# Kernel optimization log

Hardware: AMD Instinct MI355X
Metric: run time of the kernel (lower is better)

## Reference

```python
import jax, jax.numpy as jnp
import numpy as np

B, T_IN, T_OUT, C = 32, 512, 256, 64
NB_IN, NB_OUT = 16, 16
D = 128          # d_model
L = 3            # e_layers (hidden Siren layers before last)
E_IN = NB_IN * C
E_OUT = NB_OUT * C
LIN_IN = (NB_IN + 1) * C + 4
LIN_OUT = (NB_OUT + 1) * C


def _siren_params(key, E, w0_initial):
    ks = jax.random.split(key, 6)
    def unif(k, shape, std):
        return jax.random.uniform(k, shape, jnp.float32, -std, std)
    c6 = float(np.sqrt(6.0 / D))
    return dict(
        W0=unif(ks[0], (E, D, 1), 1.0),        # first layer: w_std = 1/dim_in, dim_in=1
        b0=unif(ks[1], (E, D), 1.0),
        Wh=unif(ks[2], (L - 1, E, D, D), c6),   # sqrt(6/dim)/w0, w0=1
        bh=unif(ks[3], (L - 1, E, D), c6),
        Wl=unif(ks[4], (E, 1, D), c6),
        bl=unif(ks[5], (E, 1), c6),
        w0i=w0_initial,                          # per-ensemble first-layer frequency
    )


def setup_inputs() -> dict:
    key = jax.random.key(0)
    ks = jax.random.split(key, 8)
    inp = {
        "x_enc": jax.random.normal(ks[0], (B, T_IN, C), jnp.float32),
        "x_mark_enc": jax.random.normal(ks[1], (B, T_IN, 4), jnp.float32),
        "x_dec": jax.random.normal(ks[2], (B, T_OUT, C), jnp.float32),
        "x_mark_dec": jax.random.normal(ks[3], (B, T_OUT, 4), jnp.float32),
    }
    # w0_initial: repeat(linspace(1, nb, nb), 'e -> (e c)')
    w0i_in = jnp.repeat(jnp.linspace(1.0, NB_IN, NB_IN, dtype=jnp.float32), C)
    w0i_out = jnp.repeat(jnp.linspace(1.0, NB_OUT, NB_OUT, dtype=jnp.float32), C)
    p_in = _siren_params(ks[4], E_IN, w0i_in)
    p_out = _siren_params(ks[5], E_OUT, w0i_out)
    for k, v in p_in.items():
        inp[k + "_in"] = v
    for k, v in p_out.items():
        inp[k + "_out"] = v
    std = float(1.0 / np.sqrt(LIN_IN))
    inp["Wlin"] = jax.random.uniform(ks[6], (LIN_OUT, LIN_IN), jnp.float32, -std, std)
    inp["blin"] = jax.random.uniform(ks[7], (LIN_OUT,), jnp.float32, -std, std)
    return inp


def _eigenfunc(T, nb, W0, b0, Wh, bh, Wl, bl, w0i):
    # SirenNet on domain [T,1] -> normalized eigenfunctions [T, nb+1, C]
    domain = jnp.linspace(0.0, 1.0, T, dtype=W0.dtype)[:, None]
    y = jnp.einsum('eoi,ti->teo', W0, domain) + b0           # [T,E,D]
    x = jnp.sin(w0i[None, :, None] * y)                       # Sine(w0_initial)
    for l in range(Wh.shape[0]):                              # hidden layers, w0 = 1
        x = jnp.sin(jnp.einsum('eoi,tei->teo', Wh[l], x) + bh[l])
    y = jnp.einsum('eoi,tei->teo', Wl, x) + bl                # [T,E,1], identity final act
    ef = y.reshape(T, nb, C)                                  # 't (e c) 1 -> t e c'
    ef = jnp.concatenate([jnp.ones((T, 1, C), ef.dtype), ef], axis=1)  # add_ones
    norm = jnp.sqrt(jnp.sum(ef * ef, axis=1, keepdims=True))  # normalize over basis dim
    return ef / norm


def reference(x_enc, x_mark_enc, x_dec, x_mark_dec,
              W0_in, b0_in, Wh_in, bh_in, Wl_in, bl_in, w0i_in,
              W0_out, b0_out, Wh_out, bh_out, Wl_out, bl_out, w0i_out,
              Wlin, blin):
    ef_in = _eigenfunc(T_IN, NB_IN, W0_in, b0_in, Wh_in, bh_in, Wl_in, bl_in, w0i_in)
    ef_out = _eigenfunc(T_OUT, NB_OUT, W0_out, b0_out, Wh_out, bh_out, Wl_out, bl_out, w0i_out)
    coeffs = jnp.einsum('btc,tec->bec', x_enc, ef_in)         # [B, nb+1, C]
    label = x_mark_enc[:, -1]                                  # [B, 4]
    flat = coeffs.reshape(coeffs.shape[0], -1)                 # 'b e c -> b (e c)'
    flat_in = jnp.concatenate([flat, label], axis=-1)
    pred = flat_in @ Wlin.T + blin                             # nn.Linear
    pred_coeff = pred.reshape(-1, NB_OUT + 1, C)
    pred_recon = jnp.einsum('bec,tec->btc', pred_coeff, ef_out)  # [B, pred_len, C]
    return pred_recon
```

## Files before the change

kernel.cpp:

```cpp
#include <hip/hip_runtime.h>
#include <hip/hip_bf16.h>
#include <math.h>


typedef short  bf16x8 __attribute__((ext_vector_type(8)));
typedef float  f32x4  __attribute__((ext_vector_type(4)));
typedef unsigned short u16;
typedef u16    u16x8  __attribute__((ext_vector_type(8)));
typedef unsigned int u32;
typedef u32    u32x4  __attribute__((ext_vector_type(4)));

constexpr int DD    = 128;
constexpr int E_TOT = 1024;
constexpr int T_INc = 512;
constexpr int T_OUTc= 256;
constexpr int BBc   = 32;
constexpr int CCc   = 64;
constexpr int NB1   = 17;
constexpr int EF_W  = NB1 * CCc;
constexpr int LIN_I = EF_W + 4;
constexpr int LIN_O = EF_W;

#define INV2PI 0.15915494309189535f

__device__ __forceinline__ float hsin(float rev) {
  return __builtin_amdgcn_sinf(rev);
}

__device__ __forceinline__ u32 pkrn(float a, float b) {
  __hip_bfloat162 h = __float22bfloat162_rn(float2{a, b});
  u32 r;
  __builtin_memcpy(&r, &h, 4);
  return r;
}

__device__ __forceinline__ int swz(int row, int col) {
  return row * DD + ((((col << 1) ^ ((row & 15) << 4)) >> 1));
}

__global__ __launch_bounds__(256, 4) void eigen_persist(
    const float* __restrict__ W0i, const float* __restrict__ b0i,
    const float* __restrict__ Whi, const float* __restrict__ bhi,
    const float* __restrict__ Wli, const float* __restrict__ bli,
    const float* __restrict__ w0ii, float* __restrict__ efni,
    const float* __restrict__ W0o, const float* __restrict__ b0o,
    const float* __restrict__ Who, const float* __restrict__ bho,
    const float* __restrict__ Wlo, const float* __restrict__ blo,
    const float* __restrict__ w0io, float* __restrict__ efno)
{
  __shared__ u16 xP[2][4096];
  __shared__ float yPart[4 * 32];
  __shared__ float w0s[128], b0s[128];

  const bool isIn = (blockIdx.x < E_TOT);
  const int  e    = blockIdx.x & (E_TOT - 1);
  const int  NIT  = isIn ? (T_INc / 32) : (T_OUTc / 32);
  const float tstep = isIn ? (1.0f / (float)(T_INc - 1)) : (1.0f / (float)(T_OUTc - 1));
  const float* W0 = isIn ? W0i : W0o;
  const float* b0 = isIn ? b0i : b0o;
  const float* Wh = isIn ? Whi : Who;
  const float* bh = isIn ? bhi : bho;
  const float* Wl = isIn ? Wli : Wlo;
  const float* bl = isIn ? bli : blo;
  const float* w0i = isIn ? w0ii : w0io;
  float* efn = isIn ? efni : efno;

  const int tid  = threadIdx.x;
  const int lane = tid & 63;
  const int wo   = tid >> 6;
  const int lm   = lane & 15;
  const int lg   = lane >> 4;

  const float wi  = w0i[e];
  const float blv = bl[e];

  if (tid < 128)       w0s[tid]       = W0[(size_t)e * DD + tid] * (wi * INV2PI);
  else if (tid < 256)  b0s[tid - 128] = b0[(size_t)e * DD + tid - 128] * (wi * INV2PI);

  float bhv[2][2], wlv[2];
  #pragma unroll
  for (int n = 0; n < 2; ++n) {
    const int o = wo * 32 + n * 16 + lm;
    bhv[0][n] = bh[(size_t)e * DD + o] * INV2PI;
    bhv[1][n] = bh[((size_t)E_TOT + e) * DD + o] * INV2PI;
    wlv[n]    = Wl[(size_t)e * DD + o];
  }

  bf16x8 wfrag[2][4][2];
  #pragma unroll
  for (int l = 0; l < 2; ++l) {
    const float* Wg = Wh + ((size_t)l * E_TOT + e) * (DD * DD);
    #pragma unroll
    for (int kk = 0; kk < 4; ++kk)
      #pragma unroll
      for (int n = 0; n < 2; ++n) {
        const float* p = Wg + (wo * 32 + n * 16 + lm) * DD + kk * 32 + lg * 8;
        const float4 a = *(const float4*)p;
        const float4 c = *(const float4*)(p + 4);
        u32x4 u;
        u[0] = pkrn(a.x, a.y);
        u[1] = pkrn(a.z, a.w);
        u[2] = pkrn(c.x, c.y);
        u[3] = pkrn(c.z, c.w);
        wfrag[l][kk][n] = __builtin_bit_cast(bf16x8, u);
      }
  }
  __syncthreads();

  const int tl = tid >> 3;
  const int q  = tid & 7;

  u16* x0p = xP[0];
  u16* x1p = xP[1];

  for (int it = 0; it < NIT; ++it) {
    {
      const float dom = (float)(it * 32 + tl) * tstep;
      #pragma unroll
      for (int c = 0; c < 2; ++c) {
        const int d = q * 16 + c * 8;
        const float4 wa = *(const float4*)&w0s[d];
        const float4 wb = *(const float4*)&w0s[d + 4];
        const float4 ba = *(const float4*)&b0s[d];
        const float4 bb = *(const float4*)&b0s[d + 4];
        u32x4 u;
        u[0] = pkrn(hsin(fmaf(wa.x, dom, ba.x)), hsin(fmaf(wa.y, dom, ba.y)));
        u[1] = pkrn(hsin(fmaf(wa.z, dom, ba.z)), hsin(fmaf(wa.w, dom, ba.w)));
        u[2] = pkrn(hsin(fmaf(wb.x, dom, bb.x)), hsin(fmaf(wb.y, dom, bb.y)));
        u[3] = pkrn(hsin(fmaf(wb.z, dom, bb.z)), hsin(fmaf(wb.w, dom, bb.w)));
        *(u16x8*)&x0p[swz(tl, d)] = __builtin_bit_cast(u16x8, u);
      }
    }
    __syncthreads();

    f32x4 acc[2][2];

    #pragma unroll
    for (int m = 0; m < 2; ++m)
      #pragma unroll
      for (int n = 0; n < 2; ++n) acc[m][n] = (f32x4){0.f, 0.f, 0.f, 0.f};
    #pragma unroll
    for (int kk = 0; kk < 4; ++kk) {
      const int kb = kk * 32 + lg * 8;
      bf16x8 ah[2];
      #pragma unroll
      for (int m = 0; m < 2; ++m)
        ah[m] = *(const bf16x8*)&x0p[swz(m * 16 + lm, kb)];
      #pragma unroll
      for (int m = 0; m < 2; ++m)
        #pragma unroll
        for (int n = 0; n < 2; ++n)
          acc[m][n] = __builtin_amdgcn_mfma_f32_16x16x32_bf16(ah[m], wfrag[0][kk][n], acc[m][n], 0, 0, 0);
    }
    #pragma unroll
    for (int m = 0; m < 2; ++m)
      #pragma unroll
      for (int n = 0; n < 2; ++n) {
        const int o = wo * 32 + n * 16 + lm;
        const int t = m * 16 + lg * 4;
        const u32 p0 = pkrn(hsin(fmaf(acc[m][n][0], INV2PI, bhv[0][n])),
                            hsin(fmaf(acc[m][n][1], INV2PI, bhv[0][n])));
        const u32 p1 = pkrn(hsin(fmaf(acc[m][n][2], INV2PI, bhv[0][n])),
                            hsin(fmaf(acc[m][n][3], INV2PI, bhv[0][n])));
        x1p[swz(t + 0, o)] = (u16)p0;
        x1p[swz(t + 1, o)] = (u16)(p0 >> 16);
        x1p[swz(t + 2, o)] = (u16)p1;
        x1p[swz(t + 3, o)] = (u16)(p1 >> 16);
      }
    __syncthreads();

    #pragma unroll
    for (int m = 0; m < 2; ++m)
      #pragma unroll
      for (int n = 0; n < 2; ++n) acc[m][n] = (f32x4){0.f, 0.f, 0.f, 0.f};
    #pragma unroll
    for (int kk = 0; kk < 4; ++kk) {
      const int kb = kk * 32 + lg * 8;
      bf16x8 ah[2];
      #pragma unroll
      for (int m = 0; m < 2; ++m)
        ah[m] = *(const bf16x8*)&x1p[swz(m * 16 + lm, kb)];
      #pragma unroll
      for (int m = 0; m < 2; ++m)
        #pragma unroll
        for (int n = 0; n < 2; ++n)
          acc[m][n] = __builtin_amdgcn_mfma_f32_16x16x32_bf16(ah[m], wfrag[1][kk][n], acc[m][n], 0, 0, 0);
    }

    #pragma unroll
    for (int m = 0; m < 2; ++m) {
      float p[4];
      #pragma unroll
      for (int r = 0; r < 4; ++r)
        p[r] = wlv[0] * hsin(fmaf(acc[m][0][r], INV2PI, bhv[1][0]))
             + wlv[1] * hsin(fmaf(acc[m][1][r], INV2PI, bhv[1][1]));
      #pragma unroll
      for (int r = 0; r < 4; ++r) {
        p[r] += __shfl_xor(p[r], 1);
        p[r] += __shfl_xor(p[r], 2);
        p[r] += __shfl_xor(p[r], 4);
        p[r] += __shfl_xor(p[r], 8);
      }
      if (lm == 0) {
        #pragma unroll
        for (int r = 0; r < 4; ++r)
          yPart[wo * 32 + m * 16 + lg * 4 + r] = p[r];
      }
    }
    __syncthreads();

    if (tid < 32) {
      const float s = yPart[tid] + yPart[32 + tid] + yPart[64 + tid] + yPart[96 + tid];
      efn[(size_t)(it * 32 + tid) * EF_W + CCc + e] = s + blv;
    }
  }
}

__global__ void normalize_all(float* __restrict__ efn_in, float* __restrict__ efn_out)
{
  const int tb = blockIdx.x;
  float* row = (tb < T_INc) ? (efn_in + (size_t)tb * EF_W)
                            : (efn_out + (size_t)(tb - T_INc) * EF_W);
  const int c = threadIdx.x;
  float v[16];
  float s = 1.0f;
  #pragma unroll
  for (int n = 0; n < 16; ++n) {
    v[n] = row[CCc + n * CCc + c];
    s += v[n] * v[n];
  }
  const float inv = 1.0f / sqrtf(s);
  row[c] = inv;
  #pragma unroll
  for (int n = 0; n < 16; ++n)
    row[CCc + n * CCc + c] = v[n] * inv;
}

__global__ __launch_bounds__(512) void coeffs_kernel(
    const float* __restrict__ x_enc, const float* __restrict__ x_mark_enc,
    const float* __restrict__ efn_in, float* __restrict__ flat_in)
{
  const int n  = blockIdx.x;
  const int b  = blockIdx.y;
  const int c  = threadIdx.x & 63;
  const int ch = threadIdx.x >> 6;
  __shared__ float red[8][64];
  float acc = 0.0f;
  #pragma unroll 4
  for (int t = ch * 64; t < ch * 64 + 64; ++t)
    acc += x_enc[((size_t)b * T_INc + t) * CCc + c]
         * efn_in[(size_t)t * EF_W + n * CCc + c];
  red[ch][c] = acc;
  __syncthreads();
  if (ch == 0) {
    #pragma unroll
    for (int k = 1; k < 8; ++k) acc += red[k][c];
    flat_in[b * LIN_I + n * CCc + c] = acc;
    if (n == 0 && c < 4)
      flat_in[b * LIN_I + EF_W + c] =
          x_mark_enc[((size_t)b * T_INc + (T_INc - 1)) * 4 + c];
  }
}

__global__ __launch_bounds__(256) void transpose_lin(const float* __restrict__ W,
                                                     float* __restrict__ Wt)
{
  __shared__ float tile[32][33];
  const int j0 = blockIdx.x * 32;
  const int o0 = blockIdx.y * 32;
  const int tx = threadIdx.x & 31, ty = threadIdx.x >> 5;
  #pragma unroll
  for (int r = 0; r < 32; r += 8) {
    const int o = o0 + ty + r, j = j0 + tx;
    tile[ty + r][tx] = (o < LIN_O && j < LIN_I) ? W[(size_t)o * LIN_I + j] : 0.f;
  }
  __syncthreads();
  #pragma unroll
  for (int r = 0; r < 32; r += 8) {
    const int j = j0 + ty + r, o = o0 + tx;
    if (j < LIN_I && o < LIN_O) Wt[(size_t)j * LIN_O + o] = tile[tx][ty + r];
  }
}

__global__ __launch_bounds__(256) void linear_t_kernel(
    const float* __restrict__ flat_in, const float* __restrict__ Wt,
    const float* __restrict__ blin, float* __restrict__ pred)
{
  const int og = blockIdx.x;
  const int b  = blockIdx.y;
  const int c  = threadIdx.x & 63;
  const int ch = threadIdx.x >> 6;
  const int o  = og * 64 + c;
  __shared__ float red[4][64];
  const float* xi = flat_in + b * LIN_I;
  float acc = 0.0f;
  #pragma unroll 4
  for (int j = ch * 273; j < ch * 273 + 273; ++j)
    acc += Wt[(size_t)j * LIN_O + o] * xi[j];
  red[ch][c] = acc;
  __syncthreads();
  if (ch == 0)
    pred[b * LIN_O + o] = acc + red[1][c] + red[2][c] + red[3][c] + blin[o];
}

__global__ void linear_row_kernel(const float* __restrict__ flat_in,
                                  const float* __restrict__ Wlin,
                                  const float* __restrict__ blin,
                                  float* __restrict__ pred)
{
  const int o = blockIdx.x * 64 + threadIdx.x;
  const int b = blockIdx.y;
  const float* w  = Wlin + (size_t)o * LIN_I;
  const float* xi = flat_in + b * LIN_I;
  float acc = blin[o];
  for (int j = 0; j < LIN_I; ++j) acc += w[j] * xi[j];
  pred[b * LIN_O + o] = acc;
}

__global__ void recon_kernel(const float* __restrict__ pred,
                             const float* __restrict__ efn_out,
                             float* __restrict__ out)
{
  const int b = blockIdx.y;
  const int t = blockIdx.x * 4 + (threadIdx.x >> 6);
  const int c = threadIdx.x & 63;
  float acc = 0.0f;
  #pragma unroll
  for (int n = 0; n < NB1; ++n)
    acc += pred[b * LIN_O + n * CCc + c]
         * efn_out[(size_t)t * EF_W + n * CCc + c];
  out[((size_t)b * T_OUTc + t) * CCc + c] = acc;
}

extern "C" void kernel_launch(void* const* d_in, const int* in_sizes, int n_in,
                              void* d_out, int out_size, void* d_ws, size_t ws_size,
                              hipStream_t stream)
{
  const float* x_enc      = (const float*)d_in[0];
  const float* x_mark_enc = (const float*)d_in[1];
  const float* W0_in  = (const float*)d_in[4];
  const float* b0_in  = (const float*)d_in[5];
  const float* Wh_in  = (const float*)d_in[6];
  const float* bh_in  = (const float*)d_in[7];
  const float* Wl_in  = (const float*)d_in[8];
  const float* bl_in  = (const float*)d_in[9];
  const float* w0i_in = (const float*)d_in[10];
  const float* W0_out  = (const float*)d_in[11];
  const float* b0_out  = (const float*)d_in[12];
  const float* Wh_out  = (const float*)d_in[13];
  const float* bh_out  = (const float*)d_in[14];
  const float* Wl_out  = (const float*)d_in[15];
  const float* bl_out  = (const float*)d_in[16];
  const float* w0i_out = (const float*)d_in[17];
  const float* Wlin = (const float*)d_in[18];
  const float* blin = (const float*)d_in[19];

  float* ws      = (float*)d_ws;
  float* efn_in  = ws;
  float* efn_out = efn_in + (size_t)T_INc * EF_W;
  float* flat_in = efn_out + (size_t)T_OUTc * EF_W;
  float* pred    = flat_in + (size_t)BBc * LIN_I;
  float* Wt      = pred + (size_t)BBc * LIN_O;
  const size_t needWt = ((size_t)(Wt - ws) + (size_t)LIN_I * LIN_O) * sizeof(float);
  const bool useWt = (ws_size >= needWt);

  eigen_persist<<<dim3(2 * E_TOT), dim3(256), 0, stream>>>(
      W0_in, b0_in, Wh_in, bh_in, Wl_in, bl_in, w0i_in, efn_in,
      W0_out, b0_out, Wh_out, bh_out, Wl_out, bl_out, w0i_out, efn_out);

  normalize_all<<<dim3(T_INc + T_OUTc), dim3(64), 0, stream>>>(efn_in, efn_out);

  coeffs_kernel<<<dim3(NB1, BBc), dim3(512), 0, stream>>>(x_enc, x_mark_enc, efn_in, flat_in);

  if (useWt) {
    transpose_lin<<<dim3((LIN_I + 31) / 32, (LIN_O + 31) / 32), dim3(256), 0, stream>>>(Wlin, Wt);
    linear_t_kernel<<<dim3(NB1, BBc), dim3(256), 0, stream>>>(flat_in, Wt, blin, pred);
  } else {
    linear_row_kernel<<<dim3(NB1, BBc), dim3(64), 0, stream>>>(flat_in, Wlin, blin, pred);
  }

  recon_kernel<<<dim3(T_OUTc / 4, BBc), dim3(256), 0, stream>>>(pred, efn_out, (float*)d_out);
}
```

Measured before the change: 177.4 us.

## Split eigen_persist output columns across 8 waves instead of 4

```diff
diff --git a/kernel.cpp b/kernel.cpp
--- a/kernel.cpp
+++ b/kernel.cpp
@@ -26,19 +26,17 @@
 __device__ __forceinline__ float hsin(float rev) {
   return __builtin_amdgcn_sinf(rev);
 }
-
 __device__ __forceinline__ u32 pkrn(float a, float b) {
   __hip_bfloat162 h = __float22bfloat162_rn(float2{a, b});
   u32 r;
   __builtin_memcpy(&r, &h, 4);
   return r;
 }
-
 __device__ __forceinline__ int swz(int row, int col) {
   return row * DD + ((((col << 1) ^ ((row & 15) << 4)) >> 1));
 }
 
-__global__ __launch_bounds__(256, 4) void eigen_persist(
+__global__ __launch_bounds__(512, 4) void eigen_persist(
     const float* __restrict__ W0i, const float* __restrict__ b0i,
     const float* __restrict__ Whi, const float* __restrict__ bhi,
     const float* __restrict__ Wli, const float* __restrict__ bli,
@@ -49,7 +47,7 @@
     const float* __restrict__ w0io, float* __restrict__ efno)
 {
   __shared__ u16 xP[2][4096];
-  __shared__ float yPart[4 * 32];
+  __shared__ float yPart[8 * 32];
   __shared__ float w0s[128], b0s[128];
 
   const bool isIn = (blockIdx.x < E_TOT);
@@ -70,6 +68,7 @@
   const int wo   = tid >> 6;
   const int lm   = lane & 15;
   const int lg   = lane >> 4;
+  const int o    = wo * 16 + lm;
 
   const float wi  = w0i[e];
   const float blv = bl[e];
@@ -77,38 +76,31 @@
   if (tid < 128)       w0s[tid]       = W0[(size_t)e * DD + tid] * (wi * INV2PI);
   else if (tid < 256)  b0s[tid - 128] = b0[(size_t)e * DD + tid - 128] * (wi * INV2PI);
 
-  float bhv[2][2], wlv[2];
-  #pragma unroll
-  for (int n = 0; n < 2; ++n) {
-    const int o = wo * 32 + n * 16 + lm;
-    bhv[0][n] = bh[(size_t)e * DD + o] * INV2PI;
-    bhv[1][n] = bh[((size_t)E_TOT + e) * DD + o] * INV2PI;
-    wlv[n]    = Wl[(size_t)e * DD + o];
-  }
-
-  bf16x8 wfrag[2][4][2];
+  const float bh1 = bh[(size_t)e * DD + o] * INV2PI;
+  const float bh2 = bh[((size_t)E_TOT + e) * DD + o] * INV2PI;
+  const float wlv = Wl[(size_t)e * DD + o];
+
+  bf16x8 wfrag[2][4];
   #pragma unroll
   for (int l = 0; l < 2; ++l) {
     const float* Wg = Wh + ((size_t)l * E_TOT + e) * (DD * DD);
     #pragma unroll
-    for (int kk = 0; kk < 4; ++kk)
-      #pragma unroll
-      for (int n = 0; n < 2; ++n) {
-        const float* p = Wg + (wo * 32 + n * 16 + lm) * DD + kk * 32 + lg * 8;
-        const float4 a = *(const float4*)p;
-        const float4 c = *(const float4*)(p + 4);
-        u32x4 u;
-        u[0] = pkrn(a.x, a.y);
-        u[1] = pkrn(a.z, a.w);
-        u[2] = pkrn(c.x, c.y);
-        u[3] = pkrn(c.z, c.w);
-        wfrag[l][kk][n] = __builtin_bit_cast(bf16x8, u);
-      }
+    for (int kk = 0; kk < 4; ++kk) {
+      const float* p = Wg + (size_t)o * DD + kk * 32 + lg * 8;
+      const float4 a = *(const float4*)p;
+      const float4 c = *(const float4*)(p + 4);
+      u32x4 u;
+      u[0] = pkrn(a.x, a.y);
+      u[1] = pkrn(a.z, a.w);
+      u[2] = pkrn(c.x, c.y);
+      u[3] = pkrn(c.z, c.w);
+      wfrag[l][kk] = __builtin_bit_cast(bf16x8, u);
+    }
   }
   __syncthreads();
 
-  const int tl = tid >> 3;
-  const int q  = tid & 7;
+  const int tl = tid >> 4;
+  const int q  = tid & 15;
 
   u16* x0p = xP[0];
   u16* x1p = xP[1];
@@ -116,75 +108,57 @@
   for (int it = 0; it < NIT; ++it) {
     {
       const float dom = (float)(it * 32 + tl) * tstep;
-      #pragma unroll
-      for (int c = 0; c < 2; ++c) {
-        const int d = q * 16 + c * 8;
-        const float4 wa = *(const float4*)&w0s[d];
-        const float4 wb = *(const float4*)&w0s[d + 4];
-        const float4 ba = *(const float4*)&b0s[d];
-        const float4 bb = *(const float4*)&b0s[d + 4];
-        u32x4 u;
-        u[0] = pkrn(hsin(fmaf(wa.x, dom, ba.x)), hsin(fmaf(wa.y, dom, ba.y)));
-        u[1] = pkrn(hsin(fmaf(wa.z, dom, ba.z)), hsin(fmaf(wa.w, dom, ba.w)));
-        u[2] = pkrn(hsin(fmaf(wb.x, dom, bb.x)), hsin(fmaf(wb.y, dom, bb.y)));
-        u[3] = pkrn(hsin(fmaf(wb.z, dom, bb.z)), hsin(fmaf(wb.w, dom, bb.w)));
-        *(u16x8*)&x0p[swz(tl, d)] = __builtin_bit_cast(u16x8, u);
-      }
+      const int d = q * 8;
+      const float4 wa = *(const float4*)&w0s[d];
+      const float4 wb = *(const float4*)&w0s[d + 4];
+      const float4 ba = *(const float4*)&b0s[d];
+      const float4 bb = *(const float4*)&b0s[d + 4];
+      u32x4 u;
+      u[0] = pkrn(hsin(fmaf(wa.x, dom, ba.x)), hsin(fmaf(wa.y, dom, ba.y)));
+      u[1] = pkrn(hsin(fmaf(wa.z, dom, ba.z)), hsin(fmaf(wa.w, dom, ba.w)));
+      u[2] = pkrn(hsin(fmaf(wb.x, dom, bb.x)), hsin(fmaf(wb.y, dom, bb.y)));
+      u[3] = pkrn(hsin(fmaf(wb.z, dom, bb.z)), hsin(fmaf(wb.w, dom, bb.w)));
+      *(u16x8*)&x0p[swz(tl, d)] = __builtin_bit_cast(u16x8, u);
     }
     __syncthreads();
 
-    f32x4 acc[2][2];
-
-    #pragma unroll
-    for (int m = 0; m < 2; ++m)
-      #pragma unroll
-      for (int n = 0; n < 2; ++n) acc[m][n] = (f32x4){0.f, 0.f, 0.f, 0.f};
+    f32x4 acc[2];
+
+    #pragma unroll
+    for (int m = 0; m < 2; ++m) acc[m] = (f32x4){0.f, 0.f, 0.f, 0.f};
     #pragma unroll
     for (int kk = 0; kk < 4; ++kk) {
       const int kb = kk * 32 + lg * 8;
-      bf16x8 ah[2];
-      #pragma unroll
-      for (int m = 0; m < 2; ++m)
-        ah[m] = *(const bf16x8*)&x0p[swz(m * 16 + lm, kb)];
-      #pragma unroll
-      for (int m = 0; m < 2; ++m)
-        #pragma unroll
-        for (int n = 0; n < 2; ++n)
-          acc[m][n] = __builtin_amdgcn_mfma_f32_16x16x32_bf16(ah[m], wfrag[0][kk][n], acc[m][n], 0, 0, 0);
-    }
-    #pragma unroll
-    for (int m = 0; m < 2; ++m)
-      #pragma unroll
-      for (int n = 0; n < 2; ++n) {
-        const int o = wo * 32 + n * 16 + lm;
-        const int t = m * 16 + lg * 4;
-        const u32 p0 = pkrn(hsin(fmaf(acc[m][n][0], INV2PI, bhv[0][n])),
-                            hsin(fmaf(acc[m][n][1], INV2PI, bhv[0][n])));
-        const u32 p1 = pkrn(hsin(fmaf(acc[m][n][2], INV2PI, bhv[0][n])),
-                            hsin(fmaf(acc[m][n][3], INV2PI, bhv[0][n])));
-        x1p[swz(t + 0, o)] = (u16)p0;
-        x1p[swz(t + 1, o)] = (u16)(p0 >> 16);
-        x1p[swz(t + 2, o)] = (u16)p1;
-        x1p[swz(t + 3, o)] = (u16)(p1 >> 16);
+      #pragma unroll
+      for (int m = 0; m < 2; ++m) {
+        const bf16x8 ah = *(const bf16x8*)&x0p[swz(m * 16 + lm, kb)];
+        acc[m] = __builtin_amdgcn_mfma_f32_16x16x32_bf16(ah, wfrag[0][kk], acc[m], 0, 0, 0);
       }
+    }
+    #pragma unroll
+    for (int m = 0; m < 2; ++m) {
+      const int t = m * 16 + lg * 4;
+      const u32 p0 = pkrn(hsin(fmaf(acc[m][0], INV2PI, bh1)),
+                          hsin(fmaf(acc[m][1], INV2PI, bh1)));
+      const u32 p1 = pkrn(hsin(fmaf(acc[m][2], INV2PI, bh1)),
+                          hsin(fmaf(acc[m][3], INV2PI, bh1)));
+      x1p[swz(t + 0, o)] = (u16)p0;
+      x1p[swz(t + 1, o)] = (u16)(p0 >> 16);
+      x1p[swz(t + 2, o)] = (u16)p1;
+      x1p[swz(t + 3, o)] = (u16)(p1 >> 16);
+    }
     __syncthreads();
 
     #pragma unroll
-    for (int m = 0; m < 2; ++m)
-      #pragma unroll
-      for (int n = 0; n < 2; ++n) acc[m][n] = (f32x4){0.f, 0.f, 0.f, 0.f};
+    for (int m = 0; m < 2; ++m) acc[m] = (f32x4){0.f, 0.f, 0.f, 0.f};
     #pragma unroll
     for (int kk = 0; kk < 4; ++kk) {
       const int kb = kk * 32 + lg * 8;
-      bf16x8 ah[2];
-      #pragma unroll
-      for (int m = 0; m < 2; ++m)
-        ah[m] = *(const bf16x8*)&x1p[swz(m * 16 + lm, kb)];
-      #pragma unroll
-      for (int m = 0; m < 2; ++m)
-        #pragma unroll
-        for (int n = 0; n < 2; ++n)
-          acc[m][n] = __builtin_amdgcn_mfma_f32_16x16x32_bf16(ah[m], wfrag[1][kk][n], acc[m][n], 0, 0, 0);
+      #pragma unroll
+      for (int m = 0; m < 2; ++m) {
+        const bf16x8 ah = *(const bf16x8*)&x1p[swz(m * 16 + lm, kb)];
+        acc[m] = __builtin_amdgcn_mfma_f32_16x16x32_bf16(ah, wfrag[1][kk], acc[m], 0, 0, 0);
+      }
     }
 
     #pragma unroll
@@ -192,8 +166,7 @@
       float p[4];
       #pragma unroll
       for (int r = 0; r < 4; ++r)
-        p[r] = wlv[0] * hsin(fmaf(acc[m][0][r], INV2PI, bhv[1][0]))
-             + wlv[1] * hsin(fmaf(acc[m][1][r], INV2PI, bhv[1][1]));
+        p[r] = wlv * hsin(fmaf(acc[m][r], INV2PI, bh2));
       #pragma unroll
       for (int r = 0; r < 4; ++r) {
         p[r] += __shfl_xor(p[r], 1);
@@ -210,7 +183,9 @@
     __syncthreads();
 
     if (tid < 32) {
-      const float s = yPart[tid] + yPart[32 + tid] + yPart[64 + tid] + yPart[96 + tid];
+      float s = yPart[tid];
+      #pragma unroll
+      for (int w = 1; w < 8; ++w) s += yPart[w * 32 + tid];
       efn[(size_t)(it * 32 + tid) * EF_W + CCc + e] = s + blv;
     }
   }
@@ -364,7 +339,7 @@
   const size_t needWt = ((size_t)(Wt - ws) + (size_t)LIN_I * LIN_O) * sizeof(float);
   const bool useWt = (ws_size >= needWt);
 
-  eigen_persist<<<dim3(2 * E_TOT), dim3(256), 0, stream>>>(
+  eigen_persist<<<dim3(2 * E_TOT), dim3(512), 0, stream>>>(
       W0_in, b0_in, Wh_in, bh_in, Wl_in, bl_in, w0i_in, efn_in,
       W0_out, b0_out, Wh_out, bh_out, Wl_out, bl_out, w0i_out, efn_out);
 
```

Result: slower. 214.3 us (+20.9%).
